# Optimization experiments

Hardware: AMD Instinct MI355X
Metric: run time of the kernel (lower is better)

Reference implementation:

```python
import jax, jax.numpy as jnp
import numpy as np

EMB = 128
B = 1024          # number of graphs (segments)
N = 500000        # total nodes
NEG_SLOPE = 0.01  # torch LeakyReLU default


def leaky_relu(v):
    return jnp.where(v >= 0, v, NEG_SLOPE * v)


def setup_inputs() -> dict:
    key = jax.random.key(0)
    ks = jax.random.split(key, 9)
    xg_old = jax.random.normal(ks[0], (B, EMB), dtype=jnp.float32)
    x = jax.random.normal(ks[1], (N, EMB), dtype=jnp.float32)
    batch = jnp.sort(jax.random.randint(ks[2], (N,), 0, B)).astype(jnp.int64)
    s = 1.0 / np.sqrt(EMB)
    w_mask = jax.random.uniform(ks[3], (EMB, 1), jnp.float32, -s, s)
    b_mask = jax.random.uniform(ks[4], (1,), jnp.float32, -s, s)
    w_feat = jax.random.uniform(ks[5], (EMB, EMB), jnp.float32, -s, s)
    b_feat = jax.random.uniform(ks[6], (EMB,), jnp.float32, -s, s)
    s2 = 1.0 / np.sqrt(2 * EMB)
    w_tr = jax.random.uniform(ks[7], (2 * EMB, EMB), jnp.float32, -s2, s2)
    b_tr = jax.random.uniform(ks[8], (EMB,), jnp.float32, -s2, s2)
    return {"xg_old": xg_old, "x": x, "batch": batch,
            "w_mask": w_mask, "b_mask": b_mask,
            "w_feat": w_feat, "b_feat": b_feat,
            "w_tr": w_tr, "b_tr": b_tr}


def reference(xg_old, x, batch, w_mask, b_mask, w_feat, b_feat, w_tr, b_tr):
    batch = batch.astype(jnp.int32)
    # gate score per node, segment-stable softmax over each graph
    gate = (x @ w_mask + b_mask)[:, 0]                        # [N]
    m = jax.ops.segment_max(gate, batch, num_segments=B)      # [B]
    e = jnp.exp(gate - m[batch])                              # [N]
    denom = jax.ops.segment_sum(e, batch, num_segments=B)     # [B]
    alpha = e / denom[batch]                                  # [N]
    # transformed node features, weighted segment-sum pooling
    feat = leaky_relu(x @ w_feat + b_feat)                    # [N, EMB]
    xg = jax.ops.segment_sum(alpha[:, None] * feat, batch, num_segments=B)  # [B, EMB]
    # concat with old global state, linear + LeakyReLU, residual
    cat = jnp.concatenate([xg, xg_old], axis=1)               # [B, 2*EMB]
    out = leaky_relu(cat @ w_tr + b_tr) + xg_old              # [B, EMB]
    return out
```

## Files before the change

### kernel.cpp

```cpp
#include <hip/hip_runtime.h>

typedef __attribute__((ext_vector_type(8))) short short8;
typedef __attribute__((ext_vector_type(4))) float floatx4;

__device__ __forceinline__ float b2f(unsigned int u) { return __uint_as_float(u << 16); }
__device__ __forceinline__ unsigned short f2b(float f) {
    unsigned int u = __float_as_uint(f);
    return (unsigned short)((u + 0x7fffu + ((u >> 16) & 1u)) >> 16);
}
__device__ __forceinline__ unsigned cvtpk(float lo, float hi) {
    unsigned r;
    asm("v_cvt_pk_bf16_f32 %0, %1, %2" : "=v"(r) : "v"(lo), "v"(hi));
    return r;
}

#define EMB 128
#define NN  500000
#define BB  1024
#define BM  128
#define NCT 9

__global__ __launch_bounds__(256)
void kinit(float* __restrict__ denom, float* __restrict__ xg,
           unsigned short* __restrict__ wTf, const void* __restrict__ w_feat_,
           const void* __restrict__ w_mask_, const unsigned short* __restrict__ xr,
           const int* __restrict__ braw, int* __restrict__ flags, int N)
{
    __shared__ int sf32;
    int tid = threadIdx.x;
    if (tid < 64) {
        int good = 0;
#pragma unroll
        for (int j = 0; j < 4; ++j) {
            unsigned short u = xr[tid * 4 + j];
            unsigned e = (u >> 7) & 0xffu;
            if ((e >= 100u && e <= 140u) || u == 0) ++good;
        }
#pragma unroll
        for (int o = 1; o < 64; o <<= 1) good += __shfl_xor(good, o);
        if (tid == 0) {
            sf32 = (good < 240) ? 1 : 0;
            if (blockIdx.x == 0) {
                flags[0] = sf32;
                flags[1] = (braw[N - 1] == 0 && braw[N - 2] != 0) ? 1 : 0;
            }
        }
    }
    __syncthreads();
    bool f32 = sf32 != 0;

    int i = blockIdx.x * 256 + tid;
    if (i < BB) denom[i] = 0.f;
    if (i < BB * EMB) xg[i] = 0.f;
    if (i < 4 * NCT * 512) {
        int blk = i >> 9, rem = i & 511;
        int lane = rem >> 3, j = rem & 7;
        int kk = blk / NCT, ct = blk - kk * NCT;
        int n = ct * 16 + (lane & 15);
        int k = kk * 32 + (lane >> 4) * 8 + j;
        unsigned short v = 0;
        if (n < 128)      v = f32 ? f2b(((const float*)w_feat_)[k * EMB + n])
                                  : ((const unsigned short*)w_feat_)[k * EMB + n];
        else if (n == 128) v = f32 ? f2b(((const float*)w_mask_)[k])
                                   : ((const unsigned short*)w_mask_)[k];
        wTf[i] = v;
    }
}

__global__ __launch_bounds__(256, 2)
void kmain(const void* __restrict__ x_, const int* __restrict__ braw,
           const void* __restrict__ bm_, const void* __restrict__ bf_,
           const unsigned short* __restrict__ wTf, const int* __restrict__ flags,
           float* __restrict__ denom, float* __restrict__ xg, int N)
{
    __shared__ __align__(16) unsigned short lB[4 * NCT * 512];
    __shared__ float se[BM];
    __shared__ int   sb[BM];

    int tid = threadIdx.x;
    int wave = tid >> 6, lane = tid & 63;
    int quad = lane >> 4, l16 = lane & 15;
    int woff = wave * 32;
    int n0 = blockIdx.x * BM + woff;
    bool f32  = flags[0] != 0;
    bool is64 = flags[1] != 0;

    if (lane < 32) {
        int n = n0 + lane; int s = -1;
        if (n < N) { int v = is64 ? braw[2 * n] : braw[n]; if (v >= 0 && v < BB) s = v; }
        sb[woff + lane] = s;
    }

    short8 afr[2][4];
    float4 av[16];
    if (f32) {
        const float* xf = (const float*)x_;
        float4 z = make_float4(0.f, 0.f, 0.f, 0.f);
#pragma unroll
        for (int i = 0; i < 16; ++i) av[i] = z;
#pragma unroll
        for (int rt = 0; rt < 2; ++rt) {
            int n = n0 + rt * 16 + l16;
            const float* p = xf + (size_t)n * EMB + quad * 8;
            if (n < N) {
#pragma unroll
                for (int kk = 0; kk < 4; ++kk) {
                    av[rt * 8 + kk * 2]     = *(const float4*)(p + kk * 32);
                    av[rt * 8 + kk * 2 + 1] = *(const float4*)(p + kk * 32 + 4);
                }
            }
        }
    } else {
        const unsigned short* xu = (const unsigned short*)x_;
        short8 z8 = {0, 0, 0, 0, 0, 0, 0, 0};
#pragma unroll
        for (int rt = 0; rt < 2; ++rt) {
            int n = n0 + rt * 16 + l16;
            const unsigned short* p = xu + (size_t)n * EMB + quad * 8;
#pragma unroll
            for (int kk = 0; kk < 4; ++kk) afr[rt][kk] = z8;
            if (n < N) {
#pragma unroll
                for (int kk = 0; kk < 4; ++kk)
                    afr[rt][kk] = *(const short8*)(p + kk * 32);
            }
        }
    }

    {
        const uint4* wg = (const uint4*)wTf;
        uint4* wl = (uint4*)lB;
        uint4 wv[9];
#pragma unroll
        for (int i = 0; i < 9; ++i) wv[i] = wg[i * 256 + tid];
#pragma unroll
        for (int i = 0; i < 9; ++i) wl[i * 256 + tid] = wv[i];
    }
    __syncthreads();

    if (f32) {
#pragma unroll
        for (int rt = 0; rt < 2; ++rt)
#pragma unroll
            for (int kk = 0; kk < 4; ++kk) {
                float4 a = av[rt * 8 + kk * 2], b = av[rt * 8 + kk * 2 + 1];
                union { short8 s; unsigned u[4]; } cv;
                cv.u[0] = cvtpk(a.x, a.y); cv.u[1] = cvtpk(a.z, a.w);
                cv.u[2] = cvtpk(b.x, b.y); cv.u[3] = cvtpk(b.z, b.w);
                afr[rt][kk] = cv.s;
            }
    }

    const short8* lBf = (const short8*)lB;
    floatx4 zero = {0.f, 0.f, 0.f, 0.f};
    floatx4 acc[2][NCT];
#pragma unroll
    for (int rt = 0; rt < 2; ++rt)
#pragma unroll
        for (int ct = 0; ct < NCT; ++ct) acc[rt][ct] = zero;

#pragma unroll
    for (int kk = 0; kk < 4; ++kk) {
#pragma unroll
        for (int ct = 0; ct < NCT; ++ct) {
            short8 bf = lBf[(kk * NCT + ct) * 64 + lane];
            acc[0][ct] = __builtin_amdgcn_mfma_f32_16x16x32_bf16(afr[0][kk], bf, acc[0][ct], 0, 0, 0);
            acc[1][ct] = __builtin_amdgcn_mfma_f32_16x16x32_bf16(afr[1][kk], bf, acc[1][ct], 0, 0, 0);
        }
    }

    if (l16 == 0) {
#pragma unroll
        for (int rt = 0; rt < 2; ++rt)
#pragma unroll
            for (int r = 0; r < 4; ++r)
                se[woff + rt * 16 + quad * 4 + r] = acc[rt][8][r];
    }

    float bm = f32 ? ((const float*)bm_)[0]
                   : b2f((unsigned int)((const unsigned short*)bm_)[0]);

    if (lane < 32) {
        int sv = sb[woff + lane];
        float g = se[woff + lane] + bm;
        float ev = (sv >= 0) ? __expf(fminf(g, 60.f)) : 0.f;
        se[woff + lane] = ev;
        float v = ev;
#pragma unroll
        for (int o = 1; o < 32; o <<= 1) {
            float u  = __shfl_up(v, o);
            int   su = __shfl_up(sv, o);
            if (lane >= o && su == sv) v += u;
        }
        int sn = __shfl_down(sv, 1);
        if (sv >= 0 && (lane == 31 || sn != sv)) atomicAdd(&denom[sv], v);
    }

    float bfv[8];
#pragma unroll
    for (int ct = 0; ct < 8; ++ct)
        bfv[ct] = f32 ? ((const float*)bf_)[ct * 16 + l16]
                      : b2f((unsigned int)((const unsigned short*)bf_)[ct * 16 + l16]);

    float er[2][4]; int sr[2][4];
#pragma unroll
    for (int rt = 0; rt < 2; ++rt)
#pragma unroll
        for (int r = 0; r < 4; ++r) {
            int lr = rt * 16 + quad * 4 + r;
            er[rt][r] = se[woff + lr];
            sr[rt][r] = sb[woff + lr];
        }

    int sF = sb[woff], sL = sb[woff + 31];
    if (sF == sL) {
        if (sF >= 0) {
#pragma unroll
            for (int ct = 0; ct < 8; ++ct) {
                float p = 0.f;
#pragma unroll
                for (int rt = 0; rt < 2; ++rt)
#pragma unroll
                    for (int r = 0; r < 4; ++r) {
                        float v = acc[rt][ct][r] + bfv[ct];
                        v = v >= 0.f ? v : 0.01f * v;
                        p += v * er[rt][r];
                    }
                p += __shfl_xor(p, 16);
                p += __shfl_xor(p, 32);
                if (quad == (ct & 3))
                    atomicAdd(&xg[sF * EMB + ct * 16 + l16], p);
            }
        }
    } else {
#pragma unroll
        for (int ct = 0; ct < 8; ++ct) {
            int col = ct * 16 + l16;
#pragma unroll
            for (int rt = 0; rt < 2; ++rt) {
                float a = 0.f; int cur = -1;
#pragma unroll
                for (int r = 0; r < 4; ++r) {
                    int s = sr[rt][r];
                    float v = acc[rt][ct][r] + bfv[ct];
                    v = v >= 0.f ? v : 0.01f * v;
                    v *= er[rt][r];
                    if (s != cur) {
                        if (cur >= 0) atomicAdd(&xg[cur * EMB + col], a);
                        a = 0.f; cur = s;
                    }
                    if (s >= 0) a += v;
                }
                if (cur >= 0) atomicAdd(&xg[cur * EMB + col], a);
            }
        }
    }
}

__global__ __launch_bounds__(128)
void kfinal(const float* __restrict__ xg, const float* __restrict__ denom,
            const void* __restrict__ xg_old_, const void* __restrict__ w_tr_,
            const void* __restrict__ b_tr_, const int* __restrict__ flags,
            void* __restrict__ out_)
{
    __shared__ float cat[2 * EMB];
    int b = blockIdx.x, j = threadIdx.x;
    bool f32 = flags[0] != 0;

    float d = denom[b];
    float xgv = xg[b * EMB + j];
    xgv = (d > 0.f) ? xgv / d : 0.f;
    if (xgv != xgv) xgv = 700.0f;
    cat[j] = xgv;
    float old = f32 ? ((const float*)xg_old_)[b * EMB + j]
                    : b2f((unsigned int)((const unsigned short*)xg_old_)[b * EMB + j]);
    cat[EMB + j] = old;
    __syncthreads();

    float acc = f32 ? ((const float*)b_tr_)[j]
                    : b2f((unsigned int)((const unsigned short*)b_tr_)[j]);
    if (f32) {
        const float* w = (const float*)w_tr_;
#pragma unroll 8
        for (int i = 0; i < 2 * EMB; ++i) acc = fmaf(cat[i], w[i * EMB + j], acc);
    } else {
        const unsigned short* w = (const unsigned short*)w_tr_;
#pragma unroll 8
        for (int i = 0; i < 2 * EMB; ++i) acc = fmaf(cat[i], b2f((unsigned int)w[i * EMB + j]), acc);
    }
    acc = acc >= 0.f ? acc : 0.01f * acc;
    acc += old;
    if (acc != acc) acc = 300.0f;

    if (f32) ((float*)out_)[b * EMB + j] = acc;
    else     ((unsigned short*)out_)[b * EMB + j] = f2b(acc);
}

extern "C" void kernel_launch(void* const* d_in, const int* in_sizes, int n_in,
                              void* d_out, int out_size, void* d_ws, size_t ws_size,
                              hipStream_t stream) {
    const void* xg_old = d_in[0];
    const void* x      = d_in[1];
    const int*  braw   = (const int*)d_in[2];
    const void* w_mask = d_in[3];
    const void* b_mask = d_in[4];
    const void* w_feat = d_in[5];
    const void* b_feat = d_in[6];
    const void* w_tr   = d_in[7];
    const void* b_tr   = d_in[8];

    const int N = NN;

    char* ws = (char*)d_ws;
    size_t off = 0;
    int*   flags = (int*)(ws + off);   off += 64;
    float* denom = (float*)(ws + off); off += (size_t)BB * 4;
    float* xg    = (float*)(ws + off); off += (size_t)BB * EMB * 4;
    unsigned short* wTf = (unsigned short*)(ws + off); off += (size_t)4 * NCT * 512 * 2;

    kinit<<<(BB * EMB + 255) / 256, 256, 0, stream>>>(denom, xg, wTf, w_feat, w_mask,
                                                      (const unsigned short*)x, braw, flags, N);
    kmain<<<(N + BM - 1) / BM, 256, 0, stream>>>(x, braw, b_mask, b_feat, wTf,
                                                 flags, denom, xg, N);
    kfinal<<<BB, 128, 0, stream>>>(xg, denom, xg_old, w_tr, b_tr, flags, d_out);
}
```

Measured before the change: 395.9 us.

## Make waves loop over multiple 16-row tiles with double-buffered loads

Each wave now handles CH consecutive 16-row tiles instead of one 32-row tile. The next tile's x rows and segment ids are prefetched into registers while the current tile runs its MFMA work. Weighted sums for a run of same-segment tiles stay in registers and are flushed with fewer atomics. This cuts the grid size and the per-block cost of staging weights into LDS, and lets memory loads overlap compute. In exchange it raises register pressure, with occupancy bounds now set to 3 blocks per SM, and each wave does more serial work.

```diff
diff --git a/kernel.cpp b/kernel.cpp
--- a/kernel.cpp
+++ b/kernel.cpp
@@ -17,8 +17,8 @@
 #define EMB 128
 #define NN  500000
 #define BB  1024
-#define BM  128
 #define NCT 9
+#define CH  4
 
 __global__ __launch_bounds__(256)
 void kinit(float* __restrict__ denom, float* __restrict__ xg,
@@ -67,65 +67,186 @@
     }
 }
 
-__global__ __launch_bounds__(256, 2)
+__device__ __forceinline__ void flush_racc(float (&racc)[8], int& runSeg,
+                                           int quad, int l16, float* __restrict__ xg)
+{
+    if (runSeg >= 0) {
+#pragma unroll
+        for (int ct = 0; ct < 8; ++ct) {
+            float p = racc[ct];
+            p += __shfl_xor(p, 16);
+            p += __shfl_xor(p, 32);
+            if (quad == (ct & 3))
+                atomicAdd(&xg[runSeg * EMB + ct * 16 + l16], p);
+            racc[ct] = 0.f;
+        }
+    }
+    runSeg = -1;
+}
+
+__device__ __forceinline__ void tile_compute(
+    const short8 (&afr)[4], int sv, const unsigned short* __restrict__ lB,
+    float bm, const float (&bfv)[8], float* __restrict__ sew,
+    int lane, int quad, int l16,
+    float* __restrict__ denom, float* __restrict__ xg,
+    float (&racc)[8], int& runSeg)
+{
+    const short8* lBf = (const short8*)lB;
+    floatx4 zero = {0.f, 0.f, 0.f, 0.f};
+    floatx4 acc[NCT];
+#pragma unroll
+    for (int ct = 0; ct < NCT; ++ct) acc[ct] = zero;
+
+#pragma unroll
+    for (int kk = 0; kk < 4; ++kk)
+#pragma unroll
+        for (int ct = 0; ct < NCT; ++ct) {
+            short8 bf = lBf[(kk * NCT + ct) * 64 + lane];
+            acc[ct] = __builtin_amdgcn_mfma_f32_16x16x32_bf16(afr[kk], bf, acc[ct], 0, 0, 0);
+        }
+
+    if (l16 == 0) {
+#pragma unroll
+        for (int r = 0; r < 4; ++r) sew[quad * 4 + r] = acc[8][r];
+    }
+
+    float g = sew[l16] + bm;
+    float ev = (sv >= 0) ? __expf(fminf(g, 60.f)) : 0.f;
+
+    if (lane < 16) {
+        float v = ev;
+#pragma unroll
+        for (int o = 1; o < 16; o <<= 1) {
+            float u  = __shfl_up(v, o);
+            int   su = __shfl_up(sv, o);
+            if (lane >= o && su == sv) v += u;
+        }
+        int sn = __shfl_down(sv, 1);
+        if (sv >= 0 && (lane == 15 || sn != sv)) atomicAdd(&denom[sv], v);
+    }
+
+    float er[4];
+#pragma unroll
+    for (int r = 0; r < 4; ++r) er[r] = __shfl(ev, quad * 4 + r);
+
+    int sF = __shfl(sv, 0), sL = __shfl(sv, 15);
+    if (sF == sL) {
+        if (sF >= 0) {
+            if (sF != runSeg) { flush_racc(racc, runSeg, quad, l16, xg); runSeg = sF; }
+#pragma unroll
+            for (int ct = 0; ct < 8; ++ct) {
+                float p = 0.f;
+#pragma unroll
+                for (int r = 0; r < 4; ++r) {
+                    float v = acc[ct][r] + bfv[ct];
+                    v = v >= 0.f ? v : 0.01f * v;
+                    p += v * er[r];
+                }
+                racc[ct] += p;
+            }
+        }
+    } else {
+        flush_racc(racc, runSeg, quad, l16, xg);
+        int sr[4];
+#pragma unroll
+        for (int r = 0; r < 4; ++r) sr[r] = __shfl(sv, quad * 4 + r);
+#pragma unroll
+        for (int ct = 0; ct < 8; ++ct) {
+            int col = ct * 16 + l16;
+            float a = 0.f; int cur = -1;
+#pragma unroll
+            for (int r = 0; r < 4; ++r) {
+                int s = sr[r];
+                float v = acc[ct][r] + bfv[ct];
+                v = v >= 0.f ? v : 0.01f * v;
+                v *= er[r];
+                if (s != cur) {
+                    if (cur >= 0) atomicAdd(&xg[cur * EMB + col], a);
+                    a = 0.f; cur = s;
+                }
+                if (s >= 0) a += v;
+            }
+            if (cur >= 0) atomicAdd(&xg[cur * EMB + col], a);
+        }
+    }
+}
+
+__global__ __launch_bounds__(256, 3)
 void kmain(const void* __restrict__ x_, const int* __restrict__ braw,
            const void* __restrict__ bm_, const void* __restrict__ bf_,
            const unsigned short* __restrict__ wTf, const int* __restrict__ flags,
            float* __restrict__ denom, float* __restrict__ xg, int N)
 {
     __shared__ __align__(16) unsigned short lB[4 * NCT * 512];
-    __shared__ float se[BM];
-    __shared__ int   sb[BM];
+    __shared__ float se[4][16];
 
     int tid = threadIdx.x;
     int wave = tid >> 6, lane = tid & 63;
     int quad = lane >> 4, l16 = lane & 15;
-    int woff = wave * 32;
-    int n0 = blockIdx.x * BM + woff;
     bool f32  = flags[0] != 0;
     bool is64 = flags[1] != 0;
 
-    if (lane < 32) {
-        int n = n0 + lane; int s = -1;
-        if (n < N) { int v = is64 ? braw[2 * n] : braw[n]; if (v >= 0 && v < BB) s = v; }
-        sb[woff + lane] = s;
-    }
-
-    short8 afr[2][4];
-    float4 av[16];
-    if (f32) {
-        const float* xf = (const float*)x_;
-        float4 z = make_float4(0.f, 0.f, 0.f, 0.f);
-#pragma unroll
-        for (int i = 0; i < 16; ++i) av[i] = z;
-#pragma unroll
-        for (int rt = 0; rt < 2; ++rt) {
-            int n = n0 + rt * 16 + l16;
-            const float* p = xf + (size_t)n * EMB + quad * 8;
-            if (n < N) {
-#pragma unroll
-                for (int kk = 0; kk < 4; ++kk) {
-                    av[rt * 8 + kk * 2]     = *(const float4*)(p + kk * 32);
-                    av[rt * 8 + kk * 2 + 1] = *(const float4*)(p + kk * 32 + 4);
-                }
-            }
-        }
-    } else {
-        const unsigned short* xu = (const unsigned short*)x_;
-        short8 z8 = {0, 0, 0, 0, 0, 0, 0, 0};
-#pragma unroll
-        for (int rt = 0; rt < 2; ++rt) {
-            int n = n0 + rt * 16 + l16;
-            const unsigned short* p = xu + (size_t)n * EMB + quad * 8;
-#pragma unroll
-            for (int kk = 0; kk < 4; ++kk) afr[rt][kk] = z8;
-            if (n < N) {
-#pragma unroll
-                for (int kk = 0; kk < 4; ++kk)
-                    afr[rt][kk] = *(const short8*)(p + kk * 32);
-            }
-        }
-    }
+    int T = (N + 15) >> 4;
+    int W = blockIdx.x * 4 + wave;
+    int t0 = W * CH;
+    int tend = t0 + CH; if (tend > T) tend = T;
+
+    float bm = f32 ? ((const float*)bm_)[0]
+                   : b2f((unsigned int)((const unsigned short*)bm_)[0]);
+    float bfv[8];
+#pragma unroll
+    for (int ct = 0; ct < 8; ++ct)
+        bfv[ct] = f32 ? ((const float*)bf_)[ct * 16 + l16]
+                      : b2f((unsigned int)((const unsigned short*)bf_)[ct * 16 + l16]);
+
+    float4 rA[8], rB[8];
+    short8 hA[4], hB[4];
+    int sA = -1, sB = -1;
+    const float* xf = (const float*)x_;
+    const unsigned short* xu = (const unsigned short*)x_;
+    float4 fz = make_float4(0.f, 0.f, 0.f, 0.f);
+    short8 hz = {0, 0, 0, 0, 0, 0, 0, 0};
+
+#define SEGLD(sdst, tt) do {                                                    \
+        int n_ = ((tt) << 4) + l16; int v_ = -1;                                \
+        if (n_ < N) { int b_ = is64 ? braw[2 * n_] : braw[n_];                  \
+                      if (b_ >= 0 && b_ < BB) v_ = b_; }                        \
+        sdst = v_;                                                              \
+    } while (0)
+
+#define LOADF(dst, sdst, tt) do {                                               \
+        SEGLD(sdst, tt);                                                        \
+        int n_ = ((tt) << 4) + l16;                                             \
+        const float* p_ = xf + (size_t)n_ * EMB + quad * 8;                     \
+        _Pragma("unroll")                                                       \
+        for (int kk = 0; kk < 4; ++kk) {                                        \
+            dst[kk * 2]     = (n_ < N) ? *(const float4*)(p_ + kk * 32)     : fz; \
+            dst[kk * 2 + 1] = (n_ < N) ? *(const float4*)(p_ + kk * 32 + 4) : fz; \
+        }                                                                       \
+    } while (0)
+
+#define CONVF(afr, src) do {                                                    \
+        _Pragma("unroll")                                                       \
+        for (int kk = 0; kk < 4; ++kk) {                                        \
+            float4 a_ = src[kk * 2], b_ = src[kk * 2 + 1];                      \
+            union { short8 s; unsigned u[4]; } cv_;                             \
+            cv_.u[0] = cvtpk(a_.x, a_.y); cv_.u[1] = cvtpk(a_.z, a_.w);         \
+            cv_.u[2] = cvtpk(b_.x, b_.y); cv_.u[3] = cvtpk(b_.z, b_.w);         \
+            afr[kk] = cv_.s;                                                    \
+        }                                                                       \
+    } while (0)
+
+#define LOADH(dst, sdst, tt) do {                                               \
+        SEGLD(sdst, tt);                                                        \
+        int n_ = ((tt) << 4) + l16;                                             \
+        const unsigned short* p_ = xu + (size_t)n_ * EMB + quad * 8;            \
+        _Pragma("unroll")                                                       \
+        for (int kk = 0; kk < 4; ++kk)                                          \
+            dst[kk] = (n_ < N) ? *(const short8*)(p_ + kk * 32) : hz;           \
+    } while (0)
+
+    bool havew = t0 < tend;
+    if (havew) { if (f32) LOADF(rA, sA, t0); else LOADH(hA, sA, t0); }
 
     {
         const uint4* wg = (const uint4*)wTf;
@@ -137,124 +258,56 @@
         for (int i = 0; i < 9; ++i) wl[i * 256 + tid] = wv[i];
     }
     __syncthreads();
-
+    if (!havew) return;
+
+    float racc[8];
+#pragma unroll
+    for (int ct = 0; ct < 8; ++ct) racc[ct] = 0.f;
+    int runSeg = -1;
+    float* sew = se[wave];
+
+    int t = t0;
     if (f32) {
-#pragma unroll
-        for (int rt = 0; rt < 2; ++rt)
-#pragma unroll
-            for (int kk = 0; kk < 4; ++kk) {
-                float4 a = av[rt * 8 + kk * 2], b = av[rt * 8 + kk * 2 + 1];
-                union { short8 s; unsigned u[4]; } cv;
-                cv.u[0] = cvtpk(a.x, a.y); cv.u[1] = cvtpk(a.z, a.w);
-                cv.u[2] = cvtpk(b.x, b.y); cv.u[3] = cvtpk(b.z, b.w);
-                afr[rt][kk] = cv.s;
-            }
-    }
-
-    const short8* lBf = (const short8*)lB;
-    floatx4 zero = {0.f, 0.f, 0.f, 0.f};
-    floatx4 acc[2][NCT];
-#pragma unroll
-    for (int rt = 0; rt < 2; ++rt)
-#pragma unroll
-        for (int ct = 0; ct < NCT; ++ct) acc[rt][ct] = zero;
-
-#pragma unroll
-    for (int kk = 0; kk < 4; ++kk) {
-#pragma unroll
-        for (int ct = 0; ct < NCT; ++ct) {
-            short8 bf = lBf[(kk * NCT + ct) * 64 + lane];
-            acc[0][ct] = __builtin_amdgcn_mfma_f32_16x16x32_bf16(afr[0][kk], bf, acc[0][ct], 0, 0, 0);
-            acc[1][ct] = __builtin_amdgcn_mfma_f32_16x16x32_bf16(afr[1][kk], bf, acc[1][ct], 0, 0, 0);
-        }
-    }
-
-    if (l16 == 0) {
-#pragma unroll
-        for (int rt = 0; rt < 2; ++rt)
-#pragma unroll
-            for (int r = 0; r < 4; ++r)
-                se[woff + rt * 16 + quad * 4 + r] = acc[rt][8][r];
-    }
-
-    float bm = f32 ? ((const float*)bm_)[0]
-                   : b2f((unsigned int)((const unsigned short*)bm_)[0]);
-
-    if (lane < 32) {
-        int sv = sb[woff + lane];
-        float g = se[woff + lane] + bm;
-        float ev = (sv >= 0) ? __expf(fminf(g, 60.f)) : 0.f;
-        se[woff + lane] = ev;
-        float v = ev;
-#pragma unroll
-        for (int o = 1; o < 32; o <<= 1) {
-            float u  = __shfl_up(v, o);
-            int   su = __shfl_up(sv, o);
-            if (lane >= o && su == sv) v += u;
-        }
-        int sn = __shfl_down(sv, 1);
-        if (sv >= 0 && (lane == 31 || sn != sv)) atomicAdd(&denom[sv], v);
-    }
-
-    float bfv[8];
-#pragma unroll
-    for (int ct = 0; ct < 8; ++ct)
-        bfv[ct] = f32 ? ((const float*)bf_)[ct * 16 + l16]
-                      : b2f((unsigned int)((const unsigned short*)bf_)[ct * 16 + l16]);
-
-    float er[2][4]; int sr[2][4];
-#pragma unroll
-    for (int rt = 0; rt < 2; ++rt)
-#pragma unroll
-        for (int r = 0; r < 4; ++r) {
-            int lr = rt * 16 + quad * 4 + r;
-            er[rt][r] = se[woff + lr];
-            sr[rt][r] = sb[woff + lr];
-        }
-
-    int sF = sb[woff], sL = sb[woff + 31];
-    if (sF == sL) {
-        if (sF >= 0) {
-#pragma unroll
-            for (int ct = 0; ct < 8; ++ct) {
-                float p = 0.f;
-#pragma unroll
-                for (int rt = 0; rt < 2; ++rt)
-#pragma unroll
-                    for (int r = 0; r < 4; ++r) {
-                        float v = acc[rt][ct][r] + bfv[ct];
-                        v = v >= 0.f ? v : 0.01f * v;
-                        p += v * er[rt][r];
-                    }
-                p += __shfl_xor(p, 16);
-                p += __shfl_xor(p, 32);
-                if (quad == (ct & 3))
-                    atomicAdd(&xg[sF * EMB + ct * 16 + l16], p);
+        while (true) {
+            {
+                if (t + 1 < tend) LOADF(rB, sB, t + 1);
+                short8 afr[4];
+                CONVF(afr, rA);
+                tile_compute(afr, sA, lB, bm, bfv, sew, lane, quad, l16,
+                             denom, xg, racc, runSeg);
+                ++t; if (t >= tend) break;
+            }
+            {
+                if (t + 1 < tend) LOADF(rA, sA, t + 1);
+                short8 afr[4];
+                CONVF(afr, rB);
+                tile_compute(afr, sB, lB, bm, bfv, sew, lane, quad, l16,
+                             denom, xg, racc, runSeg);
+                ++t; if (t >= tend) break;
             }
         }
     } else {
-#pragma unroll
-        for (int ct = 0; ct < 8; ++ct) {
-            int col = ct * 16 + l16;
-#pragma unroll
-            for (int rt = 0; rt < 2; ++rt) {
-                float a = 0.f; int cur = -1;
-#pragma unroll
-                for (int r = 0; r < 4; ++r) {
-                    int s = sr[rt][r];
-                    float v = acc[rt][ct][r] + bfv[ct];
-                    v = v >= 0.f ? v : 0.01f * v;
-                    v *= er[rt][r];
-                    if (s != cur) {
-                        if (cur >= 0) atomicAdd(&xg[cur * EMB + col], a);
-                        a = 0.f; cur = s;
-                    }
-                    if (s >= 0) a += v;
-                }
-                if (cur >= 0) atomicAdd(&xg[cur * EMB + col], a);
-            }
-        }
-    }
+        while (true) {
+            {
+                if (t + 1 < tend) LOADH(hB, sB, t + 1);
+                tile_compute(hA, sA, lB, bm, bfv, sew, lane, quad, l16,
+                             denom, xg, racc, runSeg);
+                ++t; if (t >= tend) break;
+            }
+            {
+                if (t + 1 < tend) LOADH(hA, sA, t + 1);
+                tile_compute(hB, sB, lB, bm, bfv, sew, lane, quad, l16,
+                             denom, xg, racc, runSeg);
+                ++t; if (t >= tend) break;
+            }
+        }
+    }
+
+    flush_racc(racc, runSeg, quad, l16, xg);
+#undef SEGLD
+#undef LOADF
+#undef CONVF
+#undef LOADH
 }
 
 __global__ __launch_bounds__(128)
@@ -318,9 +371,11 @@
     float* xg    = (float*)(ws + off); off += (size_t)BB * EMB * 4;
     unsigned short* wTf = (unsigned short*)(ws + off); off += (size_t)4 * NCT * 512 * 2;
 
+    int T = (N + 15) >> 4;
+    int nblk = (T + 4 * CH - 1) / (4 * CH);
     kinit<<<(BB * EMB + 255) / 256, 256, 0, stream>>>(denom, xg, wTf, w_feat, w_mask,
                                                       (const unsigned short*)x, braw, flags, N);
-    kmain<<<(N + BM - 1) / BM, 256, 0, stream>>>(x, braw, b_mask, b_feat, wTf,
-                                                 flags, denom, xg, N);
+    kmain<<<nblk, 256, 0, stream>>>(x, braw, b_mask, b_feat, wTf,
+                                    flags, denom, xg, N);
     kfinal<<<BB, 128, 0, stream>>>(xg, denom, xg_old, w_tr, b_tr, flags, d_out);
 }
```

Result: slower. 630.5 us (+59.3%).
